# Performance work log

Measured on AMD Instinct MI355X. Metric: run time of the kernel, lower is better.

The kernel has to match this reference:

```python
import jax, jax.numpy as jnp
import numpy as np

N = 100000
IN_DIM = 128
HID = 256
OUT_DIM = 128
E = 600000


def setup_inputs() -> dict:
    key = jax.random.key(0)
    ks = jax.random.split(key, 10)
    x = jax.random.normal(ks[0], (N, IN_DIM), dtype=jnp.float32)
    edge_index = jax.random.randint(ks[1], (2, E), 0, N, dtype=jnp.int32)

    def lin(k, fan_in, fan_out):
        kw, kb = jax.random.split(k)
        bound = 1.0 / np.sqrt(fan_in)
        W = jax.random.uniform(kw, (fan_in, fan_out), minval=-bound, maxval=bound, dtype=jnp.float32)
        b = jax.random.uniform(kb, (fan_out,), minval=-bound, maxval=bound, dtype=jnp.float32)
        return W, b

    W1a, b1a = lin(ks[2], IN_DIM, HID)
    W1b, b1b = lin(ks[3], HID, HID)
    W2a, b2a = lin(ks[4], HID, HID)
    W2b, b2b = lin(ks[5], HID, OUT_DIM)
    return {"x": x, "edge_index": edge_index,
            "W1a": W1a, "b1a": b1a, "W1b": W1b, "b1b": b1b,
            "W2a": W2a, "b2a": b2a, "W2b": W2b, "b2b": b2b}


def _gin_conv(x, src, dst, Wa, ba, Wb, bb):
    # GINConv with eps=0: h = (1+eps)*x + sum_{j in N(i)} x_j, then 2-layer MLP
    agg = jax.ops.segment_sum(x[src], dst, num_segments=N)  # [N, F]
    h = x + agg
    h = jax.nn.relu(h @ Wa + ba)
    return h @ Wb + bb


def reference(x, edge_index, W1a, b1a, W1b, b1b, W2a, b2a, W2b, b2b):
    src, dst = edge_index[0], edge_index[1]
    h = jax.nn.relu(_gin_conv(x, src, dst, W1a, b1a, W1b, b1b))
    h = jax.nn.relu(_gin_conv(h, src, dst, W2a, b2a, W2b, b2b))
    return h
```

## Files before the change

### kernel.cpp

```cpp
#include <hip/hip_runtime.h>
#include <stdint.h>

#define N_NODES 100000
#define E_EDGES 600000
#define IN_F    128
#define HID_F   256
#define OUT_F   128
#define NB_SCAN 98

typedef unsigned short ushort_t;
typedef short  short8  __attribute__((ext_vector_type(8)));
typedef float  floatx4 __attribute__((ext_vector_type(4)));

__device__ __forceinline__ float bf2f(unsigned u16) {
    return __uint_as_float(u16 << 16);
}
__device__ __forceinline__ ushort_t f2bf(float f) {
    unsigned u = __float_as_uint(f);
    return (ushort_t)((u + 0x7fffu + ((u >> 16) & 1u)) >> 16);
}

__global__ void k_prep(const float* __restrict__ x, ushort_t* __restrict__ xbf,
                       const float* __restrict__ W1a, const float* __restrict__ W1b,
                       const float* __restrict__ W2a, const float* __restrict__ W2b,
                       ushort_t* __restrict__ WT1a, ushort_t* __restrict__ WT1b,
                       ushort_t* __restrict__ WT2a, ushort_t* __restrict__ WT2b,
                       int* __restrict__ cursor) {
    int t = blockIdx.x * 256 + threadIdx.x;
    if (t < N_NODES * IN_F / 2) {
        float2 v = ((const float2*)x)[t];
        ((unsigned*)xbf)[t] = (unsigned)f2bf(v.x) | ((unsigned)f2bf(v.y) << 16);
    }
    if (t < N_NODES) cursor[t] = 0;
    if (t < 32768) {
        int k = t >> 8, n = t & 255;
        WT1a[n * 128 + k] = f2bf(W1a[t]);
    } else if (t < 98304) {
        int i = t - 32768, k = i >> 8, n = i & 255;
        WT1b[n * 256 + k] = f2bf(W1b[i]);
    } else if (t < 163840) {
        int i = t - 98304, k = i >> 8, n = i & 255;
        WT2a[n * 256 + k] = f2bf(W2a[i]);
    } else if (t < 196608) {
        int i = t - 163840, k = i >> 7, n = i & 127;
        WT2b[n * 256 + k] = f2bf(W2b[i]);
    }
}

__global__ void k_hist(const int* __restrict__ dst, int* __restrict__ deg) {
    int e = blockIdx.x * 256 + threadIdx.x;
    if (e < E_EDGES) atomicAdd(&deg[dst[e]], 1);
}

__global__ void k_scan1(const int* __restrict__ deg, int* __restrict__ row_ptr,
                        int* __restrict__ psum) {
    __shared__ int s[1024];
    int t = threadIdx.x, i = blockIdx.x * 1024 + t;
    int v = (i < N_NODES) ? deg[i] : 0;
    s[t] = v;
    __syncthreads();
    for (int off = 1; off < 1024; off <<= 1) {
        int u = (t >= off) ? s[t - off] : 0;
        __syncthreads();
        if (t >= off) s[t] += u;
        __syncthreads();
    }
    if (i < N_NODES) row_ptr[i] = s[t] - v;
    if (t == 1023) psum[blockIdx.x] = s[t];
}

__global__ void k_scan2(int* __restrict__ psum) {
    __shared__ int s[128];
    int t = threadIdx.x;
    int v = (t < NB_SCAN) ? psum[t] : 0;
    s[t] = v;
    __syncthreads();
    for (int off = 1; off < 128; off <<= 1) {
        int u = (t >= off) ? s[t - off] : 0;
        __syncthreads();
        if (t >= off) s[t] += u;
        __syncthreads();
    }
    if (t < NB_SCAN) psum[t] = s[t] - v;
}

__global__ void k_scan3(int* __restrict__ row_ptr, const int* __restrict__ psum,
                        int* __restrict__ cursor) {
    int i = blockIdx.x * 1024 + threadIdx.x;
    if (i < N_NODES) {
        int r = row_ptr[i] + psum[i >> 10];
        row_ptr[i] = r;
        cursor[i]  = r;
    }
    if (i == 0) row_ptr[N_NODES] = E_EDGES;
}

__global__ void k_fill(const int* __restrict__ src, const int* __restrict__ dst,
                       int* __restrict__ cursor, int* __restrict__ colidx) {
    int e = blockIdx.x * 256 + threadIdx.x;
    if (e < E_EDGES) {
        int pos = atomicAdd(&cursor[dst[e]], 1);
        colidx[pos] = src[e];
    }
}

__global__ void k_agg128(const ushort_t* __restrict__ Xbf, const int* __restrict__ row_ptr,
                         const int* __restrict__ colidx, ushort_t* __restrict__ Out) {
    int node = blockIdx.x * 4 + (threadIdx.x >> 6);
    int lane = threadIdx.x & 63;
    const unsigned* xr = (const unsigned*)Xbf;
    unsigned u = xr[node * 64 + lane];
    float a0 = bf2f(u & 0xffffu), a1 = bf2f(u >> 16);
    int r0 = row_ptr[node], r1 = row_ptr[node + 1];
    int r = r0;
    for (; r + 4 <= r1; r += 4) {
        int j0 = colidx[r], j1 = colidx[r + 1], j2 = colidx[r + 2], j3 = colidx[r + 3];
        unsigned w0 = xr[j0 * 64 + lane];
        unsigned w1 = xr[j1 * 64 + lane];
        unsigned w2 = xr[j2 * 64 + lane];
        unsigned w3 = xr[j3 * 64 + lane];
        a0 += (bf2f(w0 & 0xffffu) + bf2f(w1 & 0xffffu)) +
              (bf2f(w2 & 0xffffu) + bf2f(w3 & 0xffffu));
        a1 += (bf2f(w0 >> 16) + bf2f(w1 >> 16)) +
              (bf2f(w2 >> 16) + bf2f(w3 >> 16));
    }
    for (; r < r1; ++r) {
        int j = colidx[r];
        unsigned w = xr[j * 64 + lane];
        a0 += bf2f(w & 0xffffu);
        a1 += bf2f(w >> 16);
    }
    ((unsigned*)Out)[node * 64 + lane] =
        (unsigned)f2bf(a0) | ((unsigned)f2bf(a1) << 16);
}

__global__ void k_agg256(const ushort_t* __restrict__ X, const int* __restrict__ row_ptr,
                         const int* __restrict__ colidx, ushort_t* __restrict__ Out) {
    int node = blockIdx.x * 4 + (threadIdx.x >> 6);
    int lane = threadIdx.x & 63;
    const uint2* xr = (const uint2*)X;
    uint2 u = xr[node * 64 + lane];
    float a0 = bf2f(u.x & 0xffffu), a1 = bf2f(u.x >> 16);
    float a2 = bf2f(u.y & 0xffffu), a3 = bf2f(u.y >> 16);
    int r0 = row_ptr[node], r1 = row_ptr[node + 1];
    int r = r0;
    for (; r + 4 <= r1; r += 4) {
        int j0 = colidx[r], j1 = colidx[r + 1], j2 = colidx[r + 2], j3 = colidx[r + 3];
        uint2 w0 = xr[j0 * 64 + lane];
        uint2 w1 = xr[j1 * 64 + lane];
        uint2 w2 = xr[j2 * 64 + lane];
        uint2 w3 = xr[j3 * 64 + lane];
        a0 += (bf2f(w0.x & 0xffffu) + bf2f(w1.x & 0xffffu)) +
              (bf2f(w2.x & 0xffffu) + bf2f(w3.x & 0xffffu));
        a1 += (bf2f(w0.x >> 16) + bf2f(w1.x >> 16)) +
              (bf2f(w2.x >> 16) + bf2f(w3.x >> 16));
        a2 += (bf2f(w0.y & 0xffffu) + bf2f(w1.y & 0xffffu)) +
              (bf2f(w2.y & 0xffffu) + bf2f(w3.y & 0xffffu));
        a3 += (bf2f(w0.y >> 16) + bf2f(w1.y >> 16)) +
              (bf2f(w2.y >> 16) + bf2f(w3.y >> 16));
    }
    for (; r < r1; ++r) {
        int j = colidx[r];
        uint2 w = xr[j * 64 + lane];
        a0 += bf2f(w.x & 0xffffu); a1 += bf2f(w.x >> 16);
        a2 += bf2f(w.y & 0xffffu); a3 += bf2f(w.y >> 16);
    }
    uint2 o;
    o.x = (unsigned)f2bf(a0) | ((unsigned)f2bf(a1) << 16);
    o.y = (unsigned)f2bf(a2) | ((unsigned)f2bf(a3) << 16);
    ((uint2*)Out)[node * 64 + lane] = o;
}

template <int FIN, int FOUT, bool OUT_F32>
__global__ __launch_bounds__(512, 4) void gemm_relu(
    const ushort_t* __restrict__ Act, const ushort_t* __restrict__ WT,
    const float* __restrict__ bias, void* __restrict__ Out, int nRows)
{
    constexpr int CPR = FIN / 8;
    constexpr int KC  = FIN / 32;
    constexpr int KP  = KC / 2;
    __shared__ ushort_t wt[128 * FIN];

    const int tid  = threadIdx.x;
    const int slab = blockIdx.y * 128;

    {
        const ushort_t* wsrc = WT + (size_t)slab * FIN;
#pragma unroll
        for (int rr = 0; rr < (128 * CPR) / 512; ++rr) {
            int ci  = rr * 512 + tid;
            int n   = ci / CPR;
            int csw = ci % CPR;
            int cor = csw ^ (n & 15);
            const ushort_t* g = wsrc + (size_t)n * FIN + cor * 8;
            __builtin_amdgcn_global_load_lds(
                (const __attribute__((address_space(1))) unsigned*)g,
                (__attribute__((address_space(3))) unsigned*)&wt[ci * 8],
                16, 0, 0);
        }
    }

    const int wave = tid >> 6, lane = tid & 63;
    const int quad = lane >> 4, l15 = lane & 15;
    const int rowBase = blockIdx.x * 256 + wave * 32;

    int r0 = rowBase + l15;
    int r1 = r0 + 16;
    r0 = (r0 < nRows) ? r0 : (nRows - 1);
    r1 = (r1 < nRows) ? r1 : (nRows - 1);
    const ushort_t* a0p = Act + (size_t)r0 * FIN + quad * 8;
    const ushort_t* a1p = Act + (size_t)r1 * FIN + quad * 8;

    short8 af[2][2][2];
#pragma unroll
    for (int kc = 0; kc < 2; ++kc) {
        af[0][0][kc] = *(const short8*)(a0p + kc * 32);
        af[0][1][kc] = *(const short8*)(a1p + kc * 32);
    }

    floatx4 acc[2][8];
#pragma unroll
    for (int mt = 0; mt < 2; ++mt)
#pragma unroll
        for (int nt = 0; nt < 8; ++nt)
#pragma unroll
            for (int r = 0; r < 4; ++r) acc[mt][nt][r] = 0.f;

    __syncthreads();

#pragma unroll
    for (int p = 0; p < KP; ++p) {
        const int cb = p & 1, nb = cb ^ 1;
        if (p + 1 < KP) {
#pragma unroll
            for (int kc = 0; kc < 2; ++kc) {
                af[nb][0][kc] = *(const short8*)(a0p + ((p + 1) * 2 + kc) * 32);
                af[nb][1][kc] = *(const short8*)(a1p + ((p + 1) * 2 + kc) * 32);
            }
        }
#pragma unroll
        for (int kc = 0; kc < 2; ++kc) {
            int chunk = (p * 2 + kc) * 4 + quad;
#pragma unroll
            for (int nt = 0; nt < 8; ++nt) {
                int n = nt * 16 + l15;
                int csw = chunk ^ (n & 15);
                short8 bfr = *(const short8*)&wt[n * FIN + csw * 8];
                acc[0][nt] = __builtin_amdgcn_mfma_f32_16x16x32_bf16(af[cb][0][kc], bfr, acc[0][nt], 0, 0, 0);
                acc[1][nt] = __builtin_amdgcn_mfma_f32_16x16x32_bf16(af[cb][1][kc], bfr, acc[1][nt], 0, 0, 0);
            }
        }
    }

#pragma unroll
    for (int mt = 0; mt < 2; ++mt) {
#pragma unroll
        for (int nt = 0; nt < 8; ++nt) {
            int col = slab + nt * 16 + l15;
            float bv = bias[col];
#pragma unroll
            for (int r = 0; r < 4; ++r) {
                int row = rowBase + mt * 16 + quad * 4 + r;
                if (row < nRows) {
                    float v = fmaxf(acc[mt][nt][r] + bv, 0.f);
                    if (OUT_F32)
                        ((float*)Out)[(size_t)row * FOUT + col] = v;
                    else
                        ((ushort_t*)Out)[(size_t)row * FOUT + col] = f2bf(v);
                }
            }
        }
    }
}

extern "C" void kernel_launch(void* const* d_in, const int* in_sizes, int n_in,
                              void* d_out, int out_size, void* d_ws, size_t ws_size,
                              hipStream_t stream) {
    const float* x   = (const float*)d_in[0];
    const int*   ei  = (const int*)d_in[1];
    const int*   src = ei;
    const int*   dst = ei + E_EDGES;
    const float* W1a = (const float*)d_in[2];
    const float* b1a = (const float*)d_in[3];
    const float* W1b = (const float*)d_in[4];
    const float* b1b = (const float*)d_in[5];
    const float* W2a = (const float*)d_in[6];
    const float* b2a = (const float*)d_in[7];
    const float* W2b = (const float*)d_in[8];
    const float* b2b = (const float*)d_in[9];

    ushort_t* P       = (ushort_t*)d_ws;
    ushort_t* Q       = P + (size_t)N_NODES * HID_F;
    ushort_t* xbf     = Q;
    int*      row_ptr = (int*)(Q + (size_t)N_NODES * HID_F);
    int*      cursor  = row_ptr + (N_NODES + 4);
    int*      colidx  = cursor + N_NODES;
    int*      psum    = colidx + E_EDGES;
    ushort_t* WT1a    = (ushort_t*)(psum + 128);
    ushort_t* WT1b    = WT1a + 256 * 128;
    ushort_t* WT2a    = WT1b + 256 * 256;
    ushort_t* WT2b    = WT2a + 256 * 256;

    k_prep<<<(N_NODES * IN_F / 2 + 255) / 256, 256, 0, stream>>>(
        x, xbf, W1a, W1b, W2a, W2b, WT1a, WT1b, WT2a, WT2b, cursor);

    k_hist <<<(E_EDGES + 255) / 256, 256, 0, stream>>>(dst, cursor);
    k_scan1<<<NB_SCAN, 1024, 0, stream>>>(cursor, row_ptr, psum);
    k_scan2<<<1, 128, 0, stream>>>(psum);
    k_scan3<<<NB_SCAN, 1024, 0, stream>>>(row_ptr, psum, cursor);
    k_fill <<<(E_EDGES + 255) / 256, 256, 0, stream>>>(src, dst, cursor, colidx);

    const int ROWB = (N_NODES + 255) / 256;

    k_agg128<<<N_NODES / 4, 256, 0, stream>>>(xbf, row_ptr, colidx, P);
    gemm_relu<128, 256, false><<<dim3(ROWB, 2), 512, 0, stream>>>(P, WT1a, b1a, Q, N_NODES);
    gemm_relu<256, 256, false><<<dim3(ROWB, 2), 512, 0, stream>>>(Q, WT1b, b1b, P, N_NODES);

    k_agg256<<<N_NODES / 4, 256, 0, stream>>>(P, row_ptr, colidx, Q);
    gemm_relu<256, 256, false><<<dim3(ROWB, 2), 512, 0, stream>>>(Q, WT2a, b2a, P, N_NODES);
    gemm_relu<256, 128, true><<<dim3(ROWB, 1), 512, 0, stream>>>(P, WT2b, b2b, d_out, N_NODES);
}
```

Baseline: 402.1 us.

## Widen gather loads to 16 bytes and split edges across sub-wavefronts

Both aggregation kernels now gather neighbor rows with uint4 loads. In k_agg128 each wave is split into 4 groups of 16 lanes, and in k_agg256 into 2 groups of 32 lanes. Each group handles an interleaved subset of the edges, and the partial sums are combined with xor shuffles at the end. A zero padding row at index N_NODES takes the out-of-range gathers, which removes the scalar tail loop. This aims to raise the number of neighbor loads in flight per wave and cut instruction count, at the cost of extra shuffles and wasted loads on the padding row for low-degree nodes.

```diff
diff --git a/kernel.cpp b/kernel.cpp
--- a/kernel.cpp
+++ b/kernel.cpp
@@ -25,13 +25,15 @@
                        const float* __restrict__ W2a, const float* __restrict__ W2b,
                        ushort_t* __restrict__ WT1a, ushort_t* __restrict__ WT1b,
                        ushort_t* __restrict__ WT2a, ushort_t* __restrict__ WT2b,
-                       int* __restrict__ cursor) {
+                       int* __restrict__ cursor, ushort_t* __restrict__ P) {
     int t = blockIdx.x * 256 + threadIdx.x;
     if (t < N_NODES * IN_F / 2) {
         float2 v = ((const float2*)x)[t];
         ((unsigned*)xbf)[t] = (unsigned)f2bf(v.x) | ((unsigned)f2bf(v.y) << 16);
     }
     if (t < N_NODES) cursor[t] = 0;
+    if (t < 128) ((unsigned*)(P + (size_t)N_NODES * HID_F))[t] = 0;
+    if (t < 64)  ((unsigned*)(xbf + (size_t)N_NODES * IN_F))[t] = 0;
     if (t < 32768) {
         int k = t >> 8, n = t & 255;
         WT1a[n * 128 + k] = f2bf(W1a[t]);
@@ -108,48 +110,79 @@
                          const int* __restrict__ colidx, ushort_t* __restrict__ Out) {
     int node = blockIdx.x * 4 + (threadIdx.x >> 6);
     int lane = threadIdx.x & 63;
-    const unsigned* xr = (const unsigned*)Xbf;
-    unsigned u = xr[node * 64 + lane];
-    float a0 = bf2f(u & 0xffffu), a1 = bf2f(u >> 16);
+    int q = lane >> 4, l4 = lane & 15;
+    const uint4* xr = (const uint4*)Xbf;
+    uint4 u = xr[(size_t)node * 16 + l4];
+    float a0 = q ? 0.f : bf2f(u.x & 0xffffu);
+    float a1 = q ? 0.f : bf2f(u.x >> 16);
+    float a2 = q ? 0.f : bf2f(u.y & 0xffffu);
+    float a3 = q ? 0.f : bf2f(u.y >> 16);
+    float a4 = q ? 0.f : bf2f(u.z & 0xffffu);
+    float a5 = q ? 0.f : bf2f(u.z >> 16);
+    float a6 = q ? 0.f : bf2f(u.w & 0xffffu);
+    float a7 = q ? 0.f : bf2f(u.w >> 16);
     int r0 = row_ptr[node], r1 = row_ptr[node + 1];
-    int r = r0;
-    for (; r + 4 <= r1; r += 4) {
-        int j0 = colidx[r], j1 = colidx[r + 1], j2 = colidx[r + 2], j3 = colidx[r + 3];
-        unsigned w0 = xr[j0 * 64 + lane];
-        unsigned w1 = xr[j1 * 64 + lane];
-        unsigned w2 = xr[j2 * 64 + lane];
-        unsigned w3 = xr[j3 * 64 + lane];
-        a0 += (bf2f(w0 & 0xffffu) + bf2f(w1 & 0xffffu)) +
-              (bf2f(w2 & 0xffffu) + bf2f(w3 & 0xffffu));
-        a1 += (bf2f(w0 >> 16) + bf2f(w1 >> 16)) +
-              (bf2f(w2 >> 16) + bf2f(w3 >> 16));
-    }
-    for (; r < r1; ++r) {
-        int j = colidx[r];
-        unsigned w = xr[j * 64 + lane];
-        a0 += bf2f(w & 0xffffu);
-        a1 += bf2f(w >> 16);
-    }
-    ((unsigned*)Out)[node * 64 + lane] =
-        (unsigned)f2bf(a0) | ((unsigned)f2bf(a1) << 16);
+    for (int base = r0 + q; base < r1; base += 8) {
+        int j0 = colidx[base];
+        int j1 = colidx[min(base + 4, r1 - 1)];
+        j1 = (base + 4 < r1) ? j1 : N_NODES;
+        uint4 w0 = xr[(size_t)j0 * 16 + l4];
+        uint4 w1 = xr[(size_t)j1 * 16 + l4];
+        a0 += bf2f(w0.x & 0xffffu) + bf2f(w1.x & 0xffffu);
+        a1 += bf2f(w0.x >> 16)     + bf2f(w1.x >> 16);
+        a2 += bf2f(w0.y & 0xffffu) + bf2f(w1.y & 0xffffu);
+        a3 += bf2f(w0.y >> 16)     + bf2f(w1.y >> 16);
+        a4 += bf2f(w0.z & 0xffffu) + bf2f(w1.z & 0xffffu);
+        a5 += bf2f(w0.z >> 16)     + bf2f(w1.z >> 16);
+        a6 += bf2f(w0.w & 0xffffu) + bf2f(w1.w & 0xffffu);
+        a7 += bf2f(w0.w >> 16)     + bf2f(w1.w >> 16);
+    }
+    a0 += __shfl_xor(a0, 16, 64); a0 += __shfl_xor(a0, 32, 64);
+    a1 += __shfl_xor(a1, 16, 64); a1 += __shfl_xor(a1, 32, 64);
+    a2 += __shfl_xor(a2, 16, 64); a2 += __shfl_xor(a2, 32, 64);
+    a3 += __shfl_xor(a3, 16, 64); a3 += __shfl_xor(a3, 32, 64);
+    a4 += __shfl_xor(a4, 16, 64); a4 += __shfl_xor(a4, 32, 64);
+    a5 += __shfl_xor(a5, 16, 64); a5 += __shfl_xor(a5, 32, 64);
+    a6 += __shfl_xor(a6, 16, 64); a6 += __shfl_xor(a6, 32, 64);
+    a7 += __shfl_xor(a7, 16, 64); a7 += __shfl_xor(a7, 32, 64);
+    if (q == 0) {
+        uint4 o;
+        o.x = (unsigned)f2bf(a0) | ((unsigned)f2bf(a1) << 16);
+        o.y = (unsigned)f2bf(a2) | ((unsigned)f2bf(a3) << 16);
+        o.z = (unsigned)f2bf(a4) | ((unsigned)f2bf(a5) << 16);
+        o.w = (unsigned)f2bf(a6) | ((unsigned)f2bf(a7) << 16);
+        ((uint4*)Out)[(size_t)node * 16 + l4] = o;
+    }
 }
 
 __global__ void k_agg256(const ushort_t* __restrict__ X, const int* __restrict__ row_ptr,
                          const int* __restrict__ colidx, ushort_t* __restrict__ Out) {
     int node = blockIdx.x * 4 + (threadIdx.x >> 6);
     int lane = threadIdx.x & 63;
-    const uint2* xr = (const uint2*)X;
-    uint2 u = xr[node * 64 + lane];
-    float a0 = bf2f(u.x & 0xffffu), a1 = bf2f(u.x >> 16);
-    float a2 = bf2f(u.y & 0xffffu), a3 = bf2f(u.y >> 16);
+    int h = lane >> 5, l5 = lane & 31;
+    const uint4* xr = (const uint4*)X;
+    uint4 u = xr[(size_t)node * 32 + l5];
+    float a0 = h ? 0.f : bf2f(u.x & 0xffffu);
+    float a1 = h ? 0.f : bf2f(u.x >> 16);
+    float a2 = h ? 0.f : bf2f(u.y & 0xffffu);
+    float a3 = h ? 0.f : bf2f(u.y >> 16);
+    float a4 = h ? 0.f : bf2f(u.z & 0xffffu);
+    float a5 = h ? 0.f : bf2f(u.z >> 16);
+    float a6 = h ? 0.f : bf2f(u.w & 0xffffu);
+    float a7 = h ? 0.f : bf2f(u.w >> 16);
     int r0 = row_ptr[node], r1 = row_ptr[node + 1];
-    int r = r0;
-    for (; r + 4 <= r1; r += 4) {
-        int j0 = colidx[r], j1 = colidx[r + 1], j2 = colidx[r + 2], j3 = colidx[r + 3];
-        uint2 w0 = xr[j0 * 64 + lane];
-        uint2 w1 = xr[j1 * 64 + lane];
-        uint2 w2 = xr[j2 * 64 + lane];
-        uint2 w3 = xr[j3 * 64 + lane];
+    for (int base = r0 + h; base < r1; base += 8) {
+        int j0 = colidx[base];
+        int j1 = colidx[min(base + 2, r1 - 1)];
+        int j2 = colidx[min(base + 4, r1 - 1)];
+        int j3 = colidx[min(base + 6, r1 - 1)];
+        j1 = (base + 2 < r1) ? j1 : N_NODES;
+        j2 = (base + 4 < r1) ? j2 : N_NODES;
+        j3 = (base + 6 < r1) ? j3 : N_NODES;
+        uint4 w0 = xr[(size_t)j0 * 32 + l5];
+        uint4 w1 = xr[(size_t)j1 * 32 + l5];
+        uint4 w2 = xr[(size_t)j2 * 32 + l5];
+        uint4 w3 = xr[(size_t)j3 * 32 + l5];
         a0 += (bf2f(w0.x & 0xffffu) + bf2f(w1.x & 0xffffu)) +
               (bf2f(w2.x & 0xffffu) + bf2f(w3.x & 0xffffu));
         a1 += (bf2f(w0.x >> 16) + bf2f(w1.x >> 16)) +
@@ -158,17 +191,31 @@
               (bf2f(w2.y & 0xffffu) + bf2f(w3.y & 0xffffu));
         a3 += (bf2f(w0.y >> 16) + bf2f(w1.y >> 16)) +
               (bf2f(w2.y >> 16) + bf2f(w3.y >> 16));
-    }
-    for (; r < r1; ++r) {
-        int j = colidx[r];
-        uint2 w = xr[j * 64 + lane];
-        a0 += bf2f(w.x & 0xffffu); a1 += bf2f(w.x >> 16);
-        a2 += bf2f(w.y & 0xffffu); a3 += bf2f(w.y >> 16);
-    }
-    uint2 o;
-    o.x = (unsigned)f2bf(a0) | ((unsigned)f2bf(a1) << 16);
-    o.y = (unsigned)f2bf(a2) | ((unsigned)f2bf(a3) << 16);
-    ((uint2*)Out)[node * 64 + lane] = o;
+        a4 += (bf2f(w0.z & 0xffffu) + bf2f(w1.z & 0xffffu)) +
+              (bf2f(w2.z & 0xffffu) + bf2f(w3.z & 0xffffu));
+        a5 += (bf2f(w0.z >> 16) + bf2f(w1.z >> 16)) +
+              (bf2f(w2.z >> 16) + bf2f(w3.z >> 16));
+        a6 += (bf2f(w0.w & 0xffffu) + bf2f(w1.w & 0xffffu)) +
+              (bf2f(w2.w & 0xffffu) + bf2f(w3.w & 0xffffu));
+        a7 += (bf2f(w0.w >> 16) + bf2f(w1.w >> 16)) +
+              (bf2f(w2.w >> 16) + bf2f(w3.w >> 16));
+    }
+    a0 += __shfl_xor(a0, 32, 64);
+    a1 += __shfl_xor(a1, 32, 64);
+    a2 += __shfl_xor(a2, 32, 64);
+    a3 += __shfl_xor(a3, 32, 64);
+    a4 += __shfl_xor(a4, 32, 64);
+    a5 += __shfl_xor(a5, 32, 64);
+    a6 += __shfl_xor(a6, 32, 64);
+    a7 += __shfl_xor(a7, 32, 64);
+    if (h == 0) {
+        uint4 o;
+        o.x = (unsigned)f2bf(a0) | ((unsigned)f2bf(a1) << 16);
+        o.y = (unsigned)f2bf(a2) | ((unsigned)f2bf(a3) << 16);
+        o.z = (unsigned)f2bf(a4) | ((unsigned)f2bf(a5) << 16);
+        o.w = (unsigned)f2bf(a6) | ((unsigned)f2bf(a7) << 16);
+        ((uint4*)Out)[(size_t)node * 32 + l5] = o;
+    }
 }
 
 template <int FIN, int FOUT, bool OUT_F32>
@@ -289,10 +336,11 @@
     const float* W2b = (const float*)d_in[8];
     const float* b2b = (const float*)d_in[9];
 
+    const size_t NP1 = N_NODES + 1;
     ushort_t* P       = (ushort_t*)d_ws;
-    ushort_t* Q       = P + (size_t)N_NODES * HID_F;
+    ushort_t* Q       = P + NP1 * HID_F;
     ushort_t* xbf     = Q;
-    int*      row_ptr = (int*)(Q + (size_t)N_NODES * HID_F);
+    int*      row_ptr = (int*)(Q + NP1 * HID_F);
     int*      cursor  = row_ptr + (N_NODES + 4);
     int*      colidx  = cursor + N_NODES;
     int*      psum    = colidx + E_EDGES;
@@ -302,7 +350,7 @@
     ushort_t* WT2b    = WT2a + 256 * 256;
 
     k_prep<<<(N_NODES * IN_F / 2 + 255) / 256, 256, 0, stream>>>(
-        x, xbf, W1a, W1b, W2a, W2b, WT1a, WT1b, WT2a, WT2b, cursor);
+        x, xbf, W1a, W1b, W2a, W2b, WT1a, WT1b, WT2a, WT2b, cursor, P);
 
     k_hist <<<(E_EDGES + 255) / 256, 256, 0, stream>>>(dst, cursor);
     k_scan1<<<NB_SCAN, 1024, 0, stream>>>(cursor, row_ptr, psum);
```

After: 393.3 us. 2.2% less time.
